# Optimization experiments

Hardware: AMD Instinct MI355X
Metric: run time of the kernel (lower is better)

Reference implementation:

```python
import jax, jax.numpy as jnp
import numpy as np

D_MODEL = 1024
NHEAD = 16
HEAD_DIM = D_MODEL // NHEAD
D_FF = 4096
EPS = 1e-5


def _layernorm(x, g, b):
    mu = jnp.mean(x, axis=-1, keepdims=True)
    var = jnp.mean(jnp.square(x - mu), axis=-1, keepdims=True)
    return (x - mu) * jax.lax.rsqrt(var + EPS) * g + b


def setup_inputs() -> dict:
    key = jax.random.key(0)
    ks = jax.random.split(key, 8)

    def xavier(k, shape):
        fan_out, fan_in = shape
        lim = np.sqrt(6.0 / (fan_in + fan_out))
        return jax.random.uniform(k, shape, jnp.float32, -lim, lim)

    x = jax.random.normal(ks[0], (4, 2048, D_MODEL), jnp.float32)
    return {
        "x": x,
        "Wq": xavier(ks[1], (D_MODEL, D_MODEL)), "bq": jnp.zeros((D_MODEL,), jnp.float32),
        "Wk": xavier(ks[2], (D_MODEL, D_MODEL)), "bk": jnp.zeros((D_MODEL,), jnp.float32),
        "Wv": xavier(ks[3], (D_MODEL, D_MODEL)), "bv": jnp.zeros((D_MODEL,), jnp.float32),
        "Wo": xavier(ks[4], (D_MODEL, D_MODEL)), "bo": jnp.zeros((D_MODEL,), jnp.float32),
        "W1": xavier(ks[5], (D_FF, D_MODEL)), "b1": jnp.zeros((D_FF,), jnp.float32),
        "W2": xavier(ks[6], (D_MODEL, D_FF)), "b2": jnp.zeros((D_MODEL,), jnp.float32),
        "ln1_g": jnp.ones((D_MODEL,), jnp.float32), "ln1_b": jnp.zeros((D_MODEL,), jnp.float32),
        "ln2_g": jnp.ones((D_MODEL,), jnp.float32), "ln2_b": jnp.zeros((D_MODEL,), jnp.float32),
    }


def reference(x, Wq, bq, Wk, bk, Wv, bv, Wo, bo, W1, b1, W2, b2, ln1_g, ln1_b, ln2_g, ln2_b):
    B, T, D = x.shape
    H, Hd = NHEAD, HEAD_DIM

    # --- attention sublayer (pre-LN) ---
    residual = x
    xn = _layernorm(x, ln1_g, ln1_b)
    # torch Linear: y = x @ W.T + b
    q = (xn @ Wq.T + bq).reshape(B, T, H, Hd).transpose(0, 2, 1, 3)  # [B,H,T,Hd]
    k = (xn @ Wk.T + bk).reshape(B, T, H, Hd).transpose(0, 2, 1, 3)
    v = (xn @ Wv.T + bv).reshape(B, T, H, Hd).transpose(0, 2, 1, 3)

    scale = Hd ** -0.5
    scores = jnp.einsum('bhqd,bhkd->bhqk', q, k) * scale  # [B,H,T,T]
    attn = jax.nn.softmax(scores, axis=-1)
    out = jnp.einsum('bhqk,bhkd->bhqd', attn, v)           # [B,H,T,Hd]
    out = out.transpose(0, 2, 1, 3).reshape(B, T, D)
    out = out @ Wo.T + bo
    x = residual + out

    # --- FFN sublayer (pre-LN) ---
    residual = x
    xn = _layernorm(x, ln2_g, ln2_b)
    h = jax.nn.relu(xn @ W1.T + b1)
    h = h @ W2.T + b2
    return residual + h
```

## Files before the change

kernel.cpp:

```cpp
#include <hip/hip_runtime.h>
#include <hip/hip_bf16.h>

using bf16 = __hip_bfloat16;
typedef __attribute__((ext_vector_type(8))) short bf16x8;
typedef __attribute__((ext_vector_type(4))) float f32x4;

#define D_MODEL 1024
#define NHEAD 16
#define HEAD_DIM 64
#define D_FF 4096
#define SEQ 2048
#define NTOK 8192

__device__ __forceinline__ void gload16(const void* g, void* l) {
  __builtin_amdgcn_global_load_lds((const __attribute__((address_space(1))) void*)g,
                                   (__attribute__((address_space(3))) void*)l, 16, 0, 0);
}

__device__ __forceinline__ unsigned pkbf16(float lo, float hi) {
  unsigned r;
  asm("v_cvt_pk_bf16_f32 %0, %1, %2" : "=v"(r) : "v"(lo), "v"(hi));
  return r;
}

__global__ void cvt_f32_bf16(const float* __restrict__ in, bf16* __restrict__ out, int n) {
  int i = (blockIdx.x * 256 + threadIdx.x) * 4;
  if (i >= n) return;
  const float4 v = *(const float4*)&in[i];
  out[i + 0] = __float2bfloat16(v.x);
  out[i + 1] = __float2bfloat16(v.y);
  out[i + 2] = __float2bfloat16(v.z);
  out[i + 3] = __float2bfloat16(v.w);
}

__global__ __launch_bounds__(256) void layernorm_kernel(
    const float* __restrict__ xin, const float* __restrict__ g,
    const float* __restrict__ bta, bf16* __restrict__ out) {
  const int row = blockIdx.x, t = threadIdx.x;
  const float4 v = *(const float4*)&xin[(size_t)row * D_MODEL + t * 4];
  float s = v.x + v.y + v.z + v.w;
#pragma unroll
  for (int m = 1; m < 64; m <<= 1) s += __shfl_xor(s, m);
  __shared__ float red[4], red2[4];
  const int w = t >> 6, l = t & 63;
  if (l == 0) red[w] = s;
  __syncthreads();
  const float mu = (red[0] + red[1] + red[2] + red[3]) * (1.f / 1024.f);
  const float d0 = v.x - mu, d1 = v.y - mu, d2 = v.z - mu, d3 = v.w - mu;
  float q = d0 * d0 + d1 * d1 + d2 * d2 + d3 * d3;
#pragma unroll
  for (int m = 1; m < 64; m <<= 1) q += __shfl_xor(q, m);
  if (l == 0) red2[w] = q;
  __syncthreads();
  const float var = (red2[0] + red2[1] + red2[2] + red2[3]) * (1.f / 1024.f);
  const float rs = rsqrtf(var + 1e-5f);
  const float4 gg = *(const float4*)&g[t * 4];
  const float4 bb = *(const float4*)&bta[t * 4];
  bf16* o = out + (size_t)row * D_MODEL + t * 4;
  o[0] = __float2bfloat16(d0 * rs * gg.x + bb.x);
  o[1] = __float2bfloat16(d1 * rs * gg.y + bb.y);
  o[2] = __float2bfloat16(d2 * rs * gg.z + bb.z);
  o[3] = __float2bfloat16(d3 * rs * gg.w + bb.w);
}

template <int BN_, int MODE>
__global__ __launch_bounds__(512, 2) void gemm8(
    const bf16* __restrict__ A, const bf16* __restrict__ Bw,
    const float* __restrict__ bias0, const float* __restrict__ bias1,
    const float* __restrict__ bias2, const float* __restrict__ res,
    void* __restrict__ out, int M, int N, int K) {
  constexpr int NI = BN_ / 128;
  constexpr int ASZ = 256 * 128;
  constexpr int BSZ = BN_ * 128;
  constexpr int TILE = ASZ + BSZ;
  constexpr int NBL = BN_ / 64;

  __shared__ __align__(16) char smem[2 * TILE];

  const int t = threadIdx.x;
  const int l = t & 63, l15 = l & 15, l4 = l >> 4;
  const int w = t >> 6;
  const int m0 = blockIdx.y * 256, n0 = blockIdx.x * BN_;
  const int wc = w * (16 * NI);

  const int sr = t >> 3;
  const int scol = 8 * ((t & 7) ^ (sr & 7));

  const int swz = (l15 & 7) << 4;
  int coff[2];
#pragma unroll
  for (int kk = 0; kk < 2; ++kk) coff[kk] = (kk * 64 + l4 * 16) ^ swz;

#define ST_A(j, kb, buf)                                              \
  gload16(&A[(size_t)(m0 + (j) * 64 + sr) * K + (kb) + scol],         \
          (void*)(smem + (buf) * TILE + (j) * 8192 + t * 16))
#define ST_B(j, kb, buf)                                              \
  gload16(&Bw[(size_t)(n0 + (j) * 64 + sr) * K + (kb) + scol],        \
          (void*)(smem + (buf) * TILE + ASZ + (j) * 8192 + t * 16))

  f32x4 acc[16][NI] = {};
  bf16x8 bfrag[NI][2];
  const int NTm = K >> 6;

#pragma unroll
  for (int j = 0; j < NBL; ++j) ST_B(j, 0, 0);
#pragma unroll
  for (int j = 0; j < 4; ++j) ST_A(j, 0, 0);
  asm volatile("s_waitcnt vmcnt(3)" ::: "memory");
  __builtin_amdgcn_s_barrier();

#define PHASE(p)                                                                       \
  {                                                                                    \
    if ((p) == 0) {                                                                    \
      _Pragma("unroll") for (int ni = 0; ni < NI; ++ni)                                \
          _Pragma("unroll") for (int kk = 0; kk < 2; ++kk)                             \
              bfrag[ni][kk] = *(const bf16x8*)(cb + ASZ +                              \
                                               (wc + ni * 16 + l15) * 128 + coff[kk]); \
    }                                                                                  \
    bf16x8 af[2][2];                                                                   \
    _Pragma("unroll") for (int mi2 = 0; mi2 < 2; ++mi2)                                \
        _Pragma("unroll") for (int kk = 0; kk < 2; ++kk)                               \
            af[mi2][kk] = *(const bf16x8*)(cb + ((p) * 32 + mi2 * 16 + l15) * 128 +    \
                                           coff[kk]);                                  \
    if (hasNext) {                                                                     \
      if (BN_ == 256) {                                                                \
        if ((p) < 4) { ST_B((p) & 3, kbn, nb); } else { ST_A((p) - 4, kbn, nb); }      \
      } else {                                                                         \
        if ((p) < 2) { ST_B((p) & 1, kbn, nb); }                                       \
        else if ((p) < 6) { ST_A((p) - 2, kbn, nb); }                                  \
      }                                                                                \
    }                                                                                  \
    __builtin_amdgcn_s_barrier();                                                      \
    asm volatile("s_waitcnt lgkmcnt(0)" ::: "memory");                                 \
    __builtin_amdgcn_sched_barrier(0);                                                 \
    __builtin_amdgcn_s_setprio(1);                                                     \
    _Pragma("unroll") for (int ni = 0; ni < NI; ++ni)                                  \
        _Pragma("unroll") for (int mi2 = 0; mi2 < 2; ++mi2)                            \
            _Pragma("unroll") for (int kk = 0; kk < 2; ++kk)                           \
                acc[2 * (p) + mi2][ni] = __builtin_amdgcn_mfma_f32_16x16x32_bf16(      \
                    af[mi2][kk], bfrag[ni][kk], acc[2 * (p) + mi2][ni], 0, 0, 0);      \
    __builtin_amdgcn_s_setprio(0);                                                     \
    if ((p) == 1) asm volatile("s_waitcnt vmcnt(4)" ::: "memory");                     \
    if ((p) == 3) asm volatile("s_waitcnt vmcnt(5)" ::: "memory");                     \
    if ((p) == 5) asm volatile("s_waitcnt vmcnt(6)" ::: "memory");                     \
    if ((p) == 7) asm volatile("s_waitcnt vmcnt(3)" ::: "memory");                     \
    __builtin_amdgcn_s_barrier();                                                      \
  }

  for (int kt = 0; kt < NTm; ++kt) {
    const char* cb = smem + (kt & 1) * TILE;
    const int nb = (kt & 1) ^ 1;
    const int kbn = (kt + 1) << 6;
    const bool hasNext = (kt + 1 < NTm);
    PHASE(0) PHASE(1) PHASE(2) PHASE(3) PHASE(4) PHASE(5) PHASE(6) PHASE(7)
  }
#undef PHASE
#undef ST_A
#undef ST_B

#pragma unroll
  for (int mi = 0; mi < 16; ++mi) {
#pragma unroll
    for (int ni = 0; ni < NI; ++ni) {
      const int col = n0 + wc + ni * 16 + l15;
      float bb;
      if constexpr (MODE == 0) {
        const int sel = col >> 10;
        const float* bp = (sel == 0) ? bias0 : ((sel == 1) ? bias1 : bias2);
        bb = bp[col & 1023];
      } else {
        bb = bias0[col];
      }
#pragma unroll
      for (int r = 0; r < 4; ++r) {
        const int row = m0 + mi * 16 + l4 * 4 + r;
        float y = acc[mi][ni][r] + bb;
        if constexpr (MODE == 1) y = fmaxf(y, 0.f);
        if constexpr (MODE == 2) {
          y += res[(size_t)row * N + col];
          ((float*)out)[(size_t)row * N + col] = y;
        } else if constexpr (MODE == 0) {
          const int sel = col >> 10;
          const int c10 = col & 1023;
          const size_t dst = (size_t)sel * (NTOK * 1024) +
                             (size_t)((row >> 11) * NHEAD + (c10 >> 6)) * (SEQ * HEAD_DIM) +
                             (size_t)(row & (SEQ - 1)) * HEAD_DIM + (c10 & 63);
          ((bf16*)out)[dst] = __float2bfloat16(y);
        } else {
          ((bf16*)out)[(size_t)row * N + col] = __float2bfloat16(y);
        }
      }
    }
  }
}

#define SCL 0.18033688011112042f
#define NT (SEQ / 64)

__global__ __launch_bounds__(256, 2) void flash_attn(
    const bf16* __restrict__ Q, const bf16* __restrict__ K,
    const bf16* __restrict__ V, bf16* __restrict__ O) {
  __shared__ char smem[32768];
  const int t = threadIdx.x;
  const int w = t >> 6, l = t & 63;
  const int l15 = l & 15, l4 = l >> 4;
  const int bh = blockIdx.y;
  const size_t base = (size_t)bh * (SEQ * HEAD_DIM);
  const int q0 = blockIdx.x * 256 + w * 64;
  const short* Vg = (const short*)V;
  const int dV = w * 16 + l15;

  int krow[4], kswz[4];
#pragma unroll
  for (int ni = 0; ni < 4; ++ni) {
    const int kr = (ni >> 1) * 32 + (ni & 1) * 4 + (l15 >> 2) * 8 + (l15 & 3);
    krow[ni] = kr * 128;
    kswz[ni] = ((kr & 3) | (((kr >> 3) & 1) << 2)) << 4;
  }

  bf16x8 qf[4][2];
#pragma unroll
  for (int mi = 0; mi < 4; ++mi)
#pragma unroll
    for (int kk = 0; kk < 2; ++kk)
      qf[mi][kk] = *(const bf16x8*)&Q[base + (size_t)(q0 + mi * 16 + l15) * 64 + kk * 32 + l4 * 8];

  f32x4 accO[4][4] = {};
  float m_run[4], l_run[4];
#pragma unroll
  for (int mi = 0; mi < 4; ++mi) { m_run[mi] = -1e30f; l_run[mi] = 0.f; }

  short vg[16];

#define STAGE_K(bufofs, kt)                                                       \
  {                                                                               \
    _Pragma("unroll") for (int i = 0; i < 2; ++i) {                               \
      const int F = i * 256 + t;                                                  \
      const int r_ = F >> 3;                                                      \
      const int gk_ = (r_ & 3) | (((r_ >> 3) & 1) << 2);                          \
      const int c_ = 8 * ((F & 7) ^ gk_);                                         \
      gload16(&K[base + (size_t)((kt) + r_) * 64 + c_],                           \
              (void*)(smem + (bufofs) + (i * 256 + w * 64) * 16));                \
    }                                                                             \
  }

#define V_GATHER(kt)                                                              \
  {                                                                               \
    _Pragma("unroll") for (int h_ = 0; h_ < 2; ++h_)                              \
        _Pragma("unroll") for (int j_ = 0; j_ < 8; ++j_)                          \
            vg[h_ * 8 + j_] =                                                     \
        Vg[base + (size_t)((kt) + h_ * 32 + l4 * 8 + j_) * 64 + dV];              \
  }

#define VT_WRITE(bufofs)                                                          \
  {                                                                               \
    _Pragma("unroll") for (int h_ = 0; h_ < 2; ++h_) {                            \
      bf16x8 vv;                                                                  \
      _Pragma("unroll") for (int j_ = 0; j_ < 8; ++j_) vv[j_] = vg[h_ * 8 + j_];  \
      const int kb_ = (h_ * 64 + l4 * 16) ^ ((dV & 7) << 4);                      \
      *(bf16x8*)(smem + (bufofs) + dV * 128 + kb_) = vv;                          \
    }                                                                             \
  }

  STAGE_K(0, 0);
  V_GATHER(0);
  VT_WRITE(16384);
  __syncthreads();

  for (int it = 0; it < NT; ++it) {
    const int cur = it & 1;
    const char* Kb = (const char*)smem + cur * 8192;
    const char* Vb = (const char*)smem + 16384 + cur * 8192;
    const bool pre = (it + 1 < NT);
    if (pre) {
      STAGE_K((cur ^ 1) * 8192, (it + 1) * 64);
      V_GATHER((it + 1) * 64);
    }

    bf16x8 kf[2][4];
#pragma unroll
    for (int kk = 0; kk < 2; ++kk)
#pragma unroll
      for (int ni = 0; ni < 4; ++ni)
        kf[kk][ni] = *(const bf16x8*)(Kb + krow[ni] + ((kk * 64 + l4 * 16) ^ kswz[ni]));

    unsigned pw[4][8];
    float corr[4];
#pragma unroll
    for (int mi = 0; mi < 4; ++mi) {
      f32x4 s[4] = {};
      __builtin_amdgcn_s_setprio(1);
#pragma unroll
      for (int kk = 0; kk < 2; ++kk)
#pragma unroll
        for (int ni = 0; ni < 4; ++ni)
          s[ni] = __builtin_amdgcn_mfma_f32_16x16x32_bf16(kf[kk][ni], qf[mi][kk], s[ni], 0, 0, 0);
      __builtin_amdgcn_s_setprio(0);

      float mx = s[0][0];
#pragma unroll
      for (int ni = 0; ni < 4; ++ni)
#pragma unroll
        for (int r = 0; r < 4; ++r) mx = fmaxf(mx, s[ni][r]);
      mx = fmaxf(mx, __shfl_xor(mx, 16));
      mx = fmaxf(mx, __shfl_xor(mx, 32));
      const float mn = fmaxf(m_run[mi], mx * SCL);
      const float c = exp2f(m_run[mi] - mn);
      m_run[mi] = mn;
      corr[mi] = c;
      float rs = 0.f;
#pragma unroll
      for (int ni = 0; ni < 4; ++ni)
#pragma unroll
        for (int r = 0; r < 4; ++r) {
          const float p = exp2f(fmaf(s[ni][r], SCL, -mn));
          s[ni][r] = p;
          rs += p;
        }
      rs += __shfl_xor(rs, 16);
      rs += __shfl_xor(rs, 32);
      l_run[mi] = l_run[mi] * c + rs;
#pragma unroll
      for (int kk = 0; kk < 2; ++kk)
#pragma unroll
        for (int jj = 0; jj < 4; ++jj) {
          const int ni = 2 * kk + (jj >> 1);
          pw[mi][kk * 4 + jj] = pkbf16(s[ni][2 * (jj & 1)], s[ni][2 * (jj & 1) + 1]);
        }
    }

    bf16x8 vf[2][4];
#pragma unroll
    for (int kk = 0; kk < 2; ++kk)
#pragma unroll
      for (int ni = 0; ni < 4; ++ni)
        vf[kk][ni] = *(const bf16x8*)(Vb + (ni * 16 + l15) * 128 +
                                      ((kk * 64 + l4 * 16) ^ ((l15 & 7) << 4)));

#pragma unroll
    for (int mi = 0; mi < 4; ++mi) {
      const float c = corr[mi];
#pragma unroll
      for (int ni = 0; ni < 4; ++ni) accO[mi][ni] *= c;
#pragma unroll
      for (int kk = 0; kk < 2; ++kk) {
        union { unsigned u[4]; bf16x8 h; } pb;
#pragma unroll
        for (int jj = 0; jj < 4; ++jj) pb.u[jj] = pw[mi][kk * 4 + jj];
        __builtin_amdgcn_s_setprio(1);
#pragma unroll
        for (int ni = 0; ni < 4; ++ni)
          accO[mi][ni] = __builtin_amdgcn_mfma_f32_16x16x32_bf16(vf[kk][ni], pb.h, accO[mi][ni], 0, 0, 0);
        __builtin_amdgcn_s_setprio(0);
      }
    }

    if (pre) VT_WRITE(16384 + (cur ^ 1) * 8192);
    __syncthreads();
  }

  char* ob = smem + w * 8192;
#pragma unroll
  for (int mi = 0; mi < 4; ++mi) {
    const float inv = 1.f / l_run[mi];
    const int qr = mi * 16 + l15;
    const int sw = (qr & 7) << 4;
#pragma unroll
    for (int ni = 0; ni < 4; ++ni)
#pragma unroll
      for (int rr = 0; rr < 2; ++rr) {
        const unsigned pk = pkbf16(accO[mi][ni][2 * rr] * inv, accO[mi][ni][2 * rr + 1] * inv);
        *(unsigned*)(ob + qr * 128 + ((ni * 32 + l4 * 8 + 4 * rr) ^ sw)) = pk;
      }
  }
  asm volatile("s_waitcnt lgkmcnt(0)" ::: "memory");
  __builtin_amdgcn_sched_barrier(0);

  const int b = bh >> 4, h = bh & 15;
  const size_t orow = ((size_t)b * SEQ + blockIdx.x * 256 + w * 64 + l) * D_MODEL + h * HEAD_DIM;
#pragma unroll
  for (int c = 0; c < 8; ++c) {
    bf16x8 vv = *(const bf16x8*)(ob + l * 128 + ((c * 16) ^ ((l & 7) << 4)));
    *(bf16x8*)&O[orow + c * 8] = vv;
  }
}

extern "C" void kernel_launch(void* const* d_in, const int* in_sizes, int n_in,
                              void* d_out, int out_size, void* d_ws, size_t ws_size,
                              hipStream_t stream) {
  const float* x     = (const float*)d_in[0];
  const float* Wq    = (const float*)d_in[1];
  const float* bq    = (const float*)d_in[2];
  const float* Wk    = (const float*)d_in[3];
  const float* bk    = (const float*)d_in[4];
  const float* Wv    = (const float*)d_in[5];
  const float* bv    = (const float*)d_in[6];
  const float* Wo    = (const float*)d_in[7];
  const float* bo    = (const float*)d_in[8];
  const float* W1    = (const float*)d_in[9];
  const float* b1    = (const float*)d_in[10];
  const float* W2    = (const float*)d_in[11];
  const float* b2    = (const float*)d_in[12];
  const float* ln1_g = (const float*)d_in[13];
  const float* ln1_b = (const float*)d_in[14];
  const float* ln2_g = (const float*)d_in[15];
  const float* ln2_b = (const float*)d_in[16];

  const size_t MB = 1ull << 20;
  char* ws = (char*)d_ws;
  bf16* wqkv = (bf16*)(ws + 0 * MB);
  bf16* wo_b = (bf16*)(ws + 6 * MB);
  bf16* w1_b = (bf16*)(ws + 8 * MB);
  bf16* w2_b = (bf16*)(ws + 16 * MB);
  bf16* xn   = (bf16*)(ws + 24 * MB);
  bf16* qb   = (bf16*)(ws + 40 * MB);
  bf16* kbuf = (bf16*)(ws + 56 * MB);
  bf16* vb   = (bf16*)(ws + 72 * MB);
  bf16* hb   = (bf16*)(ws + 40 * MB);
  float* x1  = (float*)(ws + 104 * MB);

  cvt_f32_bf16<<<1024, 256, 0, stream>>>(Wq, wqkv, 1048576);
  cvt_f32_bf16<<<1024, 256, 0, stream>>>(Wk, wqkv + 1048576, 1048576);
  cvt_f32_bf16<<<1024, 256, 0, stream>>>(Wv, wqkv + 2097152, 1048576);
  cvt_f32_bf16<<<1024, 256, 0, stream>>>(Wo, wo_b, 1048576);
  cvt_f32_bf16<<<4096, 256, 0, stream>>>(W1, w1_b, 4194304);
  cvt_f32_bf16<<<4096, 256, 0, stream>>>(W2, w2_b, 4194304);

  layernorm_kernel<<<NTOK, 256, 0, stream>>>(x, ln1_g, ln1_b, xn);

  gemm8<256, 0><<<dim3(3072 / 256, NTOK / 256), 512, 0, stream>>>(
      xn, wqkv, bq, bk, bv, nullptr, qb, NTOK, 3072, 1024);

  flash_attn<<<dim3(SEQ / 256, 4 * NHEAD), 256, 0, stream>>>(qb, kbuf, vb, xn);

  gemm8<128, 2><<<dim3(1024 / 128, NTOK / 256), 512, 0, stream>>>(
      xn, wo_b, bo, bo, bo, x, x1, NTOK, 1024, 1024);

  layernorm_kernel<<<NTOK, 256, 0, stream>>>(x1, ln2_g, ln2_b, xn);

  gemm8<256, 1><<<dim3(D_FF / 256, NTOK / 256), 512, 0, stream>>>(
      xn, w1_b, b1, b1, b1, nullptr, hb, NTOK, D_FF, 1024);

  gemm8<128, 2><<<dim3(1024 / 128, NTOK / 256), 512, 0, stream>>>(
      hb, w2_b, b2, b2, b2, x1, d_out, NTOK, 1024, D_FF);
}
```

Measured before the change: 450.7 us.

## Restructure GEMMs into 2D warp tiling with XCD swizzle and rework flash attention

Measured after the change: 431.6 us. 4.2% less time.

```diff
diff --git a/kernel.cpp b/kernel.cpp
--- a/kernel.cpp
+++ b/kernel.cpp
@@ -63,88 +63,81 @@
   o[3] = __float2bfloat16(d3 * rs * gg.w + bb.w);
 }
 
-template <int BN_, int MODE>
-__global__ __launch_bounds__(512, 2) void gemm8(
+template <int MODE>
+__global__ __launch_bounds__(512, 2) void gemmA(
     const bf16* __restrict__ A, const bf16* __restrict__ Bw,
     const float* __restrict__ bias0, const float* __restrict__ bias1,
-    const float* __restrict__ bias2, const float* __restrict__ res,
+    const float* __restrict__ bias2,
     void* __restrict__ out, int M, int N, int K) {
-  constexpr int NI = BN_ / 128;
   constexpr int ASZ = 256 * 128;
-  constexpr int BSZ = BN_ * 128;
-  constexpr int TILE = ASZ + BSZ;
-  constexpr int NBL = BN_ / 64;
-
+  constexpr int TILE = ASZ + 256 * 128;
   __shared__ __align__(16) char smem[2 * TILE];
 
   const int t = threadIdx.x;
-  const int l = t & 63, l15 = l & 15, l4 = l >> 4;
-  const int w = t >> 6;
-  const int m0 = blockIdx.y * 256, n0 = blockIdx.x * BN_;
-  const int wc = w * (16 * NI);
+  const int l = t & 63, l15 = l & 15, l4 = (l >> 4) & 3;
+  const int w = t >> 6, wm = w >> 2, wn = w & 3;
+  const int gx = gridDim.x;
+  const int nwg = gx * gridDim.y;
+  const int bid0 = blockIdx.y * gx + blockIdx.x;
+  const int bid = (bid0 & 7) * (nwg >> 3) + (bid0 >> 3);
+  const int m0 = (bid / gx) * 256, n0 = (bid % gx) * 256;
 
   const int sr = t >> 3;
   const int scol = 8 * ((t & 7) ^ (sr & 7));
-
   const int swz = (l15 & 7) << 4;
   int coff[2];
-#pragma unroll
-  for (int kk = 0; kk < 2; ++kk) coff[kk] = (kk * 64 + l4 * 16) ^ swz;
-
-#define ST_A(j, kb, buf)                                              \
-  gload16(&A[(size_t)(m0 + (j) * 64 + sr) * K + (kb) + scol],         \
+  coff[0] = (l4 * 16) ^ swz;
+  coff[1] = (64 + l4 * 16) ^ swz;
+
+#define ST_A(j, kb, buf)                                          \
+  gload16(&A[(size_t)(m0 + (j) * 64 + sr) * K + (kb) + scol],     \
           (void*)(smem + (buf) * TILE + (j) * 8192 + t * 16))
-#define ST_B(j, kb, buf)                                              \
-  gload16(&Bw[(size_t)(n0 + (j) * 64 + sr) * K + (kb) + scol],        \
+#define ST_B(j, kb, buf)                                          \
+  gload16(&Bw[(size_t)(n0 + (j) * 64 + sr) * K + (kb) + scol],    \
           (void*)(smem + (buf) * TILE + ASZ + (j) * 8192 + t * 16))
 
-  f32x4 acc[16][NI] = {};
-  bf16x8 bfrag[NI][2];
+  f32x4 acc[8][4] = {};
   const int NTm = K >> 6;
 
-#pragma unroll
-  for (int j = 0; j < NBL; ++j) ST_B(j, 0, 0);
-#pragma unroll
-  for (int j = 0; j < 4; ++j) ST_A(j, 0, 0);
-  asm volatile("s_waitcnt vmcnt(3)" ::: "memory");
+  ST_A(0, 0, 0); ST_A(2, 0, 0);
+  ST_B(0, 0, 0); ST_B(1, 0, 0); ST_B(2, 0, 0); ST_B(3, 0, 0);
+  ST_A(1, 0, 0); ST_A(3, 0, 0);
+  asm volatile("s_waitcnt vmcnt(2)" ::: "memory");
   __builtin_amdgcn_s_barrier();
 
-#define PHASE(p)                                                                       \
-  {                                                                                    \
-    if ((p) == 0) {                                                                    \
-      _Pragma("unroll") for (int ni = 0; ni < NI; ++ni)                                \
-          _Pragma("unroll") for (int kk = 0; kk < 2; ++kk)                             \
-              bfrag[ni][kk] = *(const bf16x8*)(cb + ASZ +                              \
-                                               (wc + ni * 16 + l15) * 128 + coff[kk]); \
-    }                                                                                  \
-    bf16x8 af[2][2];                                                                   \
-    _Pragma("unroll") for (int mi2 = 0; mi2 < 2; ++mi2)                                \
-        _Pragma("unroll") for (int kk = 0; kk < 2; ++kk)                               \
-            af[mi2][kk] = *(const bf16x8*)(cb + ((p) * 32 + mi2 * 16 + l15) * 128 +    \
-                                           coff[kk]);                                  \
-    if (hasNext) {                                                                     \
-      if (BN_ == 256) {                                                                \
-        if ((p) < 4) { ST_B((p) & 3, kbn, nb); } else { ST_A((p) - 4, kbn, nb); }      \
-      } else {                                                                         \
-        if ((p) < 2) { ST_B((p) & 1, kbn, nb); }                                       \
-        else if ((p) < 6) { ST_A((p) - 2, kbn, nb); }                                  \
-      }                                                                                \
-    }                                                                                  \
-    __builtin_amdgcn_s_barrier();                                                      \
-    asm volatile("s_waitcnt lgkmcnt(0)" ::: "memory");                                 \
-    __builtin_amdgcn_sched_barrier(0);                                                 \
-    __builtin_amdgcn_s_setprio(1);                                                     \
-    _Pragma("unroll") for (int ni = 0; ni < NI; ++ni)                                  \
-        _Pragma("unroll") for (int mi2 = 0; mi2 < 2; ++mi2)                            \
-            _Pragma("unroll") for (int kk = 0; kk < 2; ++kk)                           \
-                acc[2 * (p) + mi2][ni] = __builtin_amdgcn_mfma_f32_16x16x32_bf16(      \
-                    af[mi2][kk], bfrag[ni][kk], acc[2 * (p) + mi2][ni], 0, 0, 0);      \
-    __builtin_amdgcn_s_setprio(0);                                                     \
-    if ((p) == 1) asm volatile("s_waitcnt vmcnt(4)" ::: "memory");                     \
-    if ((p) == 3) asm volatile("s_waitcnt vmcnt(5)" ::: "memory");                     \
-    if ((p) == 5) asm volatile("s_waitcnt vmcnt(6)" ::: "memory");                     \
-    if ((p) == 7) asm volatile("s_waitcnt vmcnt(3)" ::: "memory");                     \
-    __builtin_amdgcn_s_barrier();                                                      \
+#define PHASE_A(p)                                                                 \
+  {                                                                                \
+    constexpr int kk = (p) & 1;                                                    \
+    constexpr int mh = ((p) >> 1) * 4;                                             \
+    bf16x8 af[4], bf[4];                                                           \
+    _Pragma("unroll") for (int m = 0; m < 4; ++m)                                  \
+      af[m] = *(const bf16x8*)(cb + (wm * 128 + (mh + m) * 16 + l15) * 128 +       \
+                               coff[kk]);                                          \
+    _Pragma("unroll") for (int n = 0; n < 4; ++n)                                  \
+      bf[n] = *(const bf16x8*)(cb + ASZ + (wn * 64 + n * 16 + l15) * 128 +         \
+                               coff[kk]);                                          \
+    if (hasNext) {                                                                 \
+      if ((p) == 0) { ST_A(0, kbn, nb); ST_A(2, kbn, nb); }                        \
+      else if ((p) == 1) { ST_B(0, kbn, nb); ST_B(1, kbn, nb); }                   \
+      else if ((p) == 2) { ST_B(2, kbn, nb); ST_B(3, kbn, nb); }                   \
+      else { ST_A(1, kbn, nb); ST_A(3, kbn, nb); }                                 \
+    }                                                                              \
+    __builtin_amdgcn_s_barrier();                                                  \
+    asm volatile("s_waitcnt lgkmcnt(0)" ::: "memory");                             \
+    __builtin_amdgcn_sched_barrier(0);                                             \
+    __builtin_amdgcn_s_setprio(1);                                                 \
+    _Pragma("unroll") for (int m = 0; m < 4; ++m)                                  \
+      _Pragma("unroll") for (int n = 0; n < 4; ++n)                                \
+        acc[mh + m][n] = __builtin_amdgcn_mfma_f32_16x16x32_bf16(                  \
+            af[m], bf[n], acc[mh + m][n], 0, 0, 0);                                \
+    __builtin_amdgcn_s_setprio(0);                                                 \
+    if ((p) == 1) {                                                                \
+      if (hasNext) asm volatile("s_waitcnt vmcnt(4)" ::: "memory");                \
+      else asm volatile("s_waitcnt vmcnt(0)" ::: "memory");                        \
+    }                                                                              \
+    if ((p) == 3 && hasNext)                                                       \
+      asm volatile("s_waitcnt vmcnt(2)" ::: "memory");                             \
+    __builtin_amdgcn_s_barrier();                                                  \
   }
 
   for (int kt = 0; kt < NTm; ++kt) {
@@ -152,17 +145,17 @@
     const int nb = (kt & 1) ^ 1;
     const int kbn = (kt + 1) << 6;
     const bool hasNext = (kt + 1 < NTm);
-    PHASE(0) PHASE(1) PHASE(2) PHASE(3) PHASE(4) PHASE(5) PHASE(6) PHASE(7)
-  }
-#undef PHASE
+    PHASE_A(0) PHASE_A(1) PHASE_A(2) PHASE_A(3)
+  }
+#undef PHASE_A
 #undef ST_A
 #undef ST_B
 
 #pragma unroll
-  for (int mi = 0; mi < 16; ++mi) {
-#pragma unroll
-    for (int ni = 0; ni < NI; ++ni) {
-      const int col = n0 + wc + ni * 16 + l15;
+  for (int mf = 0; mf < 8; ++mf) {
+#pragma unroll
+    for (int nf = 0; nf < 4; ++nf) {
+      const int col = n0 + wn * 64 + nf * 16 + l15;
       float bb;
       if constexpr (MODE == 0) {
         const int sel = col >> 10;
@@ -173,13 +166,10 @@
       }
 #pragma unroll
       for (int r = 0; r < 4; ++r) {
-        const int row = m0 + mi * 16 + l4 * 4 + r;
-        float y = acc[mi][ni][r] + bb;
+        const int row = m0 + wm * 128 + mf * 16 + l4 * 4 + r;
+        float y = acc[mf][nf][r] + bb;
         if constexpr (MODE == 1) y = fmaxf(y, 0.f);
-        if constexpr (MODE == 2) {
-          y += res[(size_t)row * N + col];
-          ((float*)out)[(size_t)row * N + col] = y;
-        } else if constexpr (MODE == 0) {
+        if constexpr (MODE == 0) {
           const int sel = col >> 10;
           const int c10 = col & 1023;
           const size_t dst = (size_t)sel * (NTOK * 1024) +
@@ -194,19 +184,117 @@
   }
 }
 
+__global__ __launch_bounds__(512, 2) void gemmB(
+    const bf16* __restrict__ A, const bf16* __restrict__ Bw,
+    const float* __restrict__ bias, const float* __restrict__ res,
+    float* __restrict__ out, int M, int N, int K) {
+  constexpr int ASZ = 128 * 128;
+  constexpr int TILE = ASZ + 256 * 128;
+  __shared__ __align__(16) char smem[3 * TILE];
+
+  const int t = threadIdx.x;
+  const int l = t & 63, l15 = l & 15, l4 = (l >> 4) & 3;
+  const int w = t >> 6, wm = w >> 2, wn = w & 3;
+  const int gx = gridDim.x;
+  const int nwg = gx * gridDim.y;
+  const int bid0 = blockIdx.y * gx + blockIdx.x;
+  const int bid = (bid0 & 7) * (nwg >> 3) + (bid0 >> 3);
+  const int m0 = (bid / gx) * 128, n0 = (bid % gx) * 256;
+
+  const int sr = t >> 3;
+  const int scol = 8 * ((t & 7) ^ (sr & 7));
+  const int swz = (l15 & 7) << 4;
+  int coff[2];
+  coff[0] = (l4 * 16) ^ swz;
+  coff[1] = (64 + l4 * 16) ^ swz;
+
+#define ST_A(j, kb, buf)                                          \
+  gload16(&A[(size_t)(m0 + (j) * 64 + sr) * K + (kb) + scol],     \
+          (void*)(smem + (buf) * TILE + (j) * 8192 + t * 16))
+#define ST_B(j, kb, buf)                                          \
+  gload16(&Bw[(size_t)(n0 + (j) * 64 + sr) * K + (kb) + scol],    \
+          (void*)(smem + (buf) * TILE + ASZ + (j) * 8192 + t * 16))
+
+  f32x4 acc[4][4] = {};
+  const int NTm = K >> 6;
+
+  ST_B(0, 0, 0); ST_B(1, 0, 0); ST_B(2, 0, 0);
+  ST_B(3, 0, 0); ST_A(0, 0, 0); ST_A(1, 0, 0);
+  ST_B(0, 64, 1); ST_B(1, 64, 1); ST_B(2, 64, 1);
+  ST_B(3, 64, 1); ST_A(0, 64, 1); ST_A(1, 64, 1);
+  asm volatile("s_waitcnt vmcnt(6)" ::: "memory");
+  __builtin_amdgcn_s_barrier();
+
+#define PHASE_B(p)                                                                 \
+  {                                                                                \
+    constexpr int kk = (p);                                                        \
+    bf16x8 af[4], bf[4];                                                           \
+    _Pragma("unroll") for (int m = 0; m < 4; ++m)                                  \
+      af[m] = *(const bf16x8*)(cb + (wm * 64 + m * 16 + l15) * 128 + coff[kk]);    \
+    _Pragma("unroll") for (int n = 0; n < 4; ++n)                                  \
+      bf[n] = *(const bf16x8*)(cb + ASZ + (wn * 64 + n * 16 + l15) * 128 +         \
+                               coff[kk]);                                          \
+    if (iss) {                                                                     \
+      if ((p) == 0) { ST_B(0, kbn, nb); ST_B(1, kbn, nb); ST_B(2, kbn, nb); }      \
+      else { ST_B(3, kbn, nb); ST_A(0, kbn, nb); ST_A(1, kbn, nb); }               \
+    }                                                                              \
+    __builtin_amdgcn_s_barrier();                                                  \
+    asm volatile("s_waitcnt lgkmcnt(0)" ::: "memory");                             \
+    __builtin_amdgcn_sched_barrier(0);                                             \
+    __builtin_amdgcn_s_setprio(1);                                                 \
+    _Pragma("unroll") for (int m = 0; m < 4; ++m)                                  \
+      _Pragma("unroll") for (int n = 0; n < 4; ++n)                                \
+        acc[m][n] = __builtin_amdgcn_mfma_f32_16x16x32_bf16(                       \
+            af[m], bf[n], acc[m][n], 0, 0, 0);                                     \
+    __builtin_amdgcn_s_setprio(0);                                                 \
+    if ((p) == 1) {                                                                \
+      if (iss) asm volatile("s_waitcnt vmcnt(6)" ::: "memory");                    \
+      else asm volatile("s_waitcnt vmcnt(0)" ::: "memory");                        \
+    }                                                                              \
+    __builtin_amdgcn_s_barrier();                                                  \
+  }
+
+  for (int kt = 0; kt < NTm; ++kt) {
+    const char* cb = smem + (kt % 3) * TILE;
+    const int nb = (kt + 2) % 3;
+    const int kbn = (kt + 2) << 6;
+    const bool iss = (kt + 2 < NTm);
+    PHASE_B(0) PHASE_B(1)
+  }
+#undef PHASE_B
+#undef ST_A
+#undef ST_B
+
+#pragma unroll
+  for (int mf = 0; mf < 4; ++mf) {
+#pragma unroll
+    for (int nf = 0; nf < 4; ++nf) {
+      const int col = n0 + wn * 64 + nf * 16 + l15;
+      const float bb = bias[col];
+#pragma unroll
+      for (int r = 0; r < 4; ++r) {
+        const int row = m0 + wm * 64 + mf * 16 + l4 * 4 + r;
+        out[(size_t)row * N + col] = acc[mf][nf][r] + bb + res[(size_t)row * N + col];
+      }
+    }
+  }
+}
+
 #define SCL 0.18033688011112042f
 #define NT (SEQ / 64)
 
-__global__ __launch_bounds__(256, 2) void flash_attn(
+__global__ __launch_bounds__(256, 4) void flash_attn(
     const bf16* __restrict__ Q, const bf16* __restrict__ K,
     const bf16* __restrict__ V, bf16* __restrict__ O) {
   __shared__ char smem[32768];
   const int t = threadIdx.x;
   const int w = t >> 6, l = t & 63;
   const int l15 = l & 15, l4 = l >> 4;
-  const int bh = blockIdx.y;
+  const int bid0 = blockIdx.y * 16 + blockIdx.x;
+  const int bid = (bid0 & 7) * 128 + (bid0 >> 3);
+  const int bx = bid & 15, bh = bid >> 4;
   const size_t base = (size_t)bh * (SEQ * HEAD_DIM);
-  const int q0 = blockIdx.x * 256 + w * 64;
+  const int q0 = bx * 128 + w * 32;
   const short* Vg = (const short*)V;
   const int dV = w * 16 + l15;
 
@@ -218,17 +306,21 @@
     kswz[ni] = ((kr & 3) | (((kr >> 3) & 1) << 2)) << 4;
   }
 
-  bf16x8 qf[4][2];
-#pragma unroll
-  for (int mi = 0; mi < 4; ++mi)
+  bf16x8 qf[2][2];
+#pragma unroll
+  for (int mi = 0; mi < 2; ++mi)
 #pragma unroll
     for (int kk = 0; kk < 2; ++kk)
       qf[mi][kk] = *(const bf16x8*)&Q[base + (size_t)(q0 + mi * 16 + l15) * 64 + kk * 32 + l4 * 8];
 
-  f32x4 accO[4][4] = {};
-  float m_run[4], l_run[4];
-#pragma unroll
-  for (int mi = 0; mi < 4; ++mi) { m_run[mi] = -1e30f; l_run[mi] = 0.f; }
+  bf16x8 ones;
+#pragma unroll
+  for (int j = 0; j < 8; ++j) ones[j] = (short)0x3F80;
+
+  f32x4 accO[2][4] = {};
+  float m_run[2], l_run[2];
+#pragma unroll
+  for (int mi = 0; mi < 2; ++mi) { m_run[mi] = -1e30f; l_run[mi] = 0.f; }
 
   short vg[16];
 
@@ -284,10 +376,9 @@
       for (int ni = 0; ni < 4; ++ni)
         kf[kk][ni] = *(const bf16x8*)(Kb + krow[ni] + ((kk * 64 + l4 * 16) ^ kswz[ni]));
 
-    unsigned pw[4][8];
-    float corr[4];
-#pragma unroll
-    for (int mi = 0; mi < 4; ++mi) {
+    unsigned pw[2][8];
+#pragma unroll
+    for (int mi = 0; mi < 2; ++mi) {
       f32x4 s[4] = {};
       __builtin_amdgcn_s_setprio(1);
 #pragma unroll
@@ -304,22 +395,22 @@
         for (int r = 0; r < 4; ++r) mx = fmaxf(mx, s[ni][r]);
       mx = fmaxf(mx, __shfl_xor(mx, 16));
       mx = fmaxf(mx, __shfl_xor(mx, 32));
-      const float mn = fmaxf(m_run[mi], mx * SCL);
-      const float c = exp2f(m_run[mi] - mn);
-      m_run[mi] = mn;
-      corr[mi] = c;
-      float rs = 0.f;
+      const float mxs = mx * SCL;
+      if (__any(mxs > m_run[mi] + 8.f)) {
+        const float mn = fmaxf(m_run[mi], mxs);
+        const float c = exp2f(m_run[mi] - mn);
+        m_run[mi] = mn;
+        l_run[mi] *= c;
+#pragma unroll
+        for (int ni = 0; ni < 4; ++ni)
+#pragma unroll
+          for (int r = 0; r < 4; ++r) accO[mi][ni][r] *= c;
+      }
 #pragma unroll
       for (int ni = 0; ni < 4; ++ni)
 #pragma unroll
-        for (int r = 0; r < 4; ++r) {
-          const float p = exp2f(fmaf(s[ni][r], SCL, -mn));
-          s[ni][r] = p;
-          rs += p;
-        }
-      rs += __shfl_xor(rs, 16);
-      rs += __shfl_xor(rs, 32);
-      l_run[mi] = l_run[mi] * c + rs;
+        for (int r = 0; r < 4; ++r)
+          s[ni][r] = exp2f(fmaf(s[ni][r], SCL, -m_run[mi]));
 #pragma unroll
       for (int kk = 0; kk < 2; ++kk)
 #pragma unroll
@@ -329,39 +420,37 @@
         }
     }
 
-    bf16x8 vf[2][4];
-#pragma unroll
-    for (int kk = 0; kk < 2; ++kk)
+    f32x4 zz[2] = {};
+#pragma unroll
+    for (int kk = 0; kk < 2; ++kk) {
+      bf16x8 vf[4];
 #pragma unroll
       for (int ni = 0; ni < 4; ++ni)
-        vf[kk][ni] = *(const bf16x8*)(Vb + (ni * 16 + l15) * 128 +
-                                      ((kk * 64 + l4 * 16) ^ ((l15 & 7) << 4)));
-
-#pragma unroll
-    for (int mi = 0; mi < 4; ++mi) {
-      const float c = corr[mi];
-#pragma unroll
-      for (int ni = 0; ni < 4; ++ni) accO[mi][ni] *= c;
-#pragma unroll
-      for (int kk = 0; kk < 2; ++kk) {
+        vf[ni] = *(const bf16x8*)(Vb + (ni * 16 + l15) * 128 +
+                                  ((kk * 64 + l4 * 16) ^ ((l15 & 7) << 4)));
+#pragma unroll
+      for (int mi = 0; mi < 2; ++mi) {
         union { unsigned u[4]; bf16x8 h; } pb;
 #pragma unroll
         for (int jj = 0; jj < 4; ++jj) pb.u[jj] = pw[mi][kk * 4 + jj];
         __builtin_amdgcn_s_setprio(1);
 #pragma unroll
         for (int ni = 0; ni < 4; ++ni)
-          accO[mi][ni] = __builtin_amdgcn_mfma_f32_16x16x32_bf16(vf[kk][ni], pb.h, accO[mi][ni], 0, 0, 0);
+          accO[mi][ni] = __builtin_amdgcn_mfma_f32_16x16x32_bf16(vf[ni], pb.h, accO[mi][ni], 0, 0, 0);
+        zz[mi] = __builtin_amdgcn_mfma_f32_16x16x32_bf16(ones, pb.h, zz[mi], 0, 0, 0);
         __builtin_amdgcn_s_setprio(0);
       }
     }
+#pragma unroll
+    for (int mi = 0; mi < 2; ++mi) l_run[mi] += zz[mi][0];
 
     if (pre) VT_WRITE(16384 + (cur ^ 1) * 8192);
     __syncthreads();
   }
 
-  char* ob = smem + w * 8192;
-#pragma unroll
-  for (int mi = 0; mi < 4; ++mi) {
+  char* ob = smem + w * 4096;
+#pragma unroll
+  for (int mi = 0; mi < 2; ++mi) {
     const float inv = 1.f / l_run[mi];
     const int qr = mi * 16 + l15;
     const int sw = (qr & 7) << 4;
@@ -377,10 +466,11 @@
   __builtin_amdgcn_sched_barrier(0);
 
   const int b = bh >> 4, h = bh & 15;
-  const size_t orow = ((size_t)b * SEQ + blockIdx.x * 256 + w * 64 + l) * D_MODEL + h * HEAD_DIM;
-#pragma unroll
-  for (int c = 0; c < 8; ++c) {
-    bf16x8 vv = *(const bf16x8*)(ob + l * 128 + ((c * 16) ^ ((l & 7) << 4)));
+  const int hr = l >> 1, hf = l & 1;
+  const size_t orow = ((size_t)b * SEQ + bx * 128 + w * 32 + hr) * D_MODEL + h * HEAD_DIM + hf * 32;
+#pragma unroll
+  for (int c = 0; c < 4; ++c) {
+    bf16x8 vv = *(const bf16x8*)(ob + hr * 128 + (((hf * 64) + c * 16) ^ ((hr & 7) << 4)));
     *(bf16x8*)&O[orow + c * 8] = vv;
   }
 }
@@ -428,19 +518,19 @@
 
   layernorm_kernel<<<NTOK, 256, 0, stream>>>(x, ln1_g, ln1_b, xn);
 
-  gemm8<256, 0><<<dim3(3072 / 256, NTOK / 256), 512, 0, stream>>>(
-      xn, wqkv, bq, bk, bv, nullptr, qb, NTOK, 3072, 1024);
-
-  flash_attn<<<dim3(SEQ / 256, 4 * NHEAD), 256, 0, stream>>>(qb, kbuf, vb, xn);
-
-  gemm8<128, 2><<<dim3(1024 / 128, NTOK / 256), 512, 0, stream>>>(
-      xn, wo_b, bo, bo, bo, x, x1, NTOK, 1024, 1024);
+  gemmA<0><<<dim3(3072 / 256, NTOK / 256), 512, 0, stream>>>(
+      xn, wqkv, bq, bk, bv, qb, NTOK, 3072, 1024);
+
+  flash_attn<<<dim3(SEQ / 128, 4 * NHEAD), 256, 0, stream>>>(qb, kbuf, vb, xn);
+
+  gemmB<<<dim3(1024 / 256, NTOK / 128), 512, 0, stream>>>(
+      xn, wo_b, bo, x, x1, NTOK, 1024, 1024);
 
   layernorm_kernel<<<NTOK, 256, 0, stream>>>(x1, ln2_g, ln2_b, xn);
 
-  gemm8<256, 1><<<dim3(D_FF / 256, NTOK / 256), 512, 0, stream>>>(
-      xn, w1_b, b1, b1, b1, nullptr, hb, NTOK, D_FF, 1024);
-
-  gemm8<128, 2><<<dim3(1024 / 128, NTOK / 256), 512, 0, stream>>>(
-      hb, w2_b, b2, b2, b2, x1, d_out, NTOK, 1024, D_FF);
-}
+  gemmA<1><<<dim3(D_FF / 256, NTOK / 256), 512, 0, stream>>>(
+      xn, w1_b, b1, b1, b1, hb, NTOK, D_FF, 1024);
+
+  gemmB<<<dim3(1024 / 256, NTOK / 128), 512, 0, stream>>>(
+      hb, w2_b, b2, x1, (float*)d_out, NTOK, 1024, D_FF);
+}
```
